# Optimization experiments

Hardware: AMD Instinct MI355X
Metric: run time of the kernel (lower is better)

## Reference

```python
import jax, jax.numpy as jnp
import numpy as np

SEQ, D, H, P, FINAL = 2048, 1024, 16, 64, 1024


def setup_inputs() -> dict:
    key = jax.random.key(0)
    k_x, k_q, k_k, k_v, k_w = jax.random.split(key, 5)
    return {
        "x": jax.random.normal(k_x, (SEQ, D), dtype=jnp.float32),
        "Qw": jax.random.uniform(k_q, (H, D, P), dtype=jnp.float32),
        "Kw": jax.random.uniform(k_k, (H, D, P), dtype=jnp.float32),
        "Vw": jax.random.uniform(k_v, (H, D, P), dtype=jnp.float32),
        "W_fin": jax.random.normal(k_w, (H * P, FINAL), dtype=jnp.float32) * (1.0 / np.sqrt(H * P)),
        "b_fin": jnp.zeros((FINAL,), dtype=jnp.float32),
    }


def reference(x, Qw, Kw, Vw, W_fin, b_fin):
    # x: [S, D]; Qw/Kw/Vw: [H, D, P]
    Q = jnp.einsum("sd,hdp->hsp", x, Qw)  # [H, S, P]
    K = jnp.einsum("sd,hdp->hsp", x, Kw)
    V = jnp.einsum("sd,hdp->hsp", x, Vw)
    p_dim = K.shape[-1]
    # sigmoid attention: no row-wise normalization, scale by P (not sqrt(P))
    score = jax.nn.sigmoid(jnp.einsum("hsp,htp->hst", Q, K) / p_dim)  # [H, S, S]
    attn = jnp.einsum("hst,htp->hsp", score, V)  # [H, S, P]
    # faithful raw reshape (torch .reshape(seq, -1) on contiguous [H, S, P])
    concat = attn.reshape(x.shape[0], -1)  # [S, H*P]
    return concat @ W_fin + b_fin  # [S, FINAL]
```

## Files before the change

### kernel.cpp

```cpp
#include <hip/hip_runtime.h>
#include <hip/hip_bf16.h>

#define SEQL 2048
#define DMODEL 1024
#define NH 16
#define HEADP 64
#define FINALD 1024

using bf16x8 = __attribute__((ext_vector_type(8))) short;
using f32x4  = __attribute__((ext_vector_type(4))) float;
using s16x4  = __attribute__((ext_vector_type(4))) short;

#define WAITV(N) asm volatile("s_waitcnt vmcnt(" #N ")" ::: "memory")

__device__ __forceinline__ f32x4 mfma16(bf16x8 a, bf16x8 b, f32x4 c) {
  return __builtin_amdgcn_mfma_f32_16x16x32_bf16(a, b, c, 0, 0, 0);
}

__device__ __forceinline__ unsigned short f2bf(float f) {
  return __builtin_bit_cast(unsigned short, __float2bfloat16(f));
}

__device__ __forceinline__ void gload16(const void* g, void* l) {
  __builtin_amdgcn_global_load_lds(
      (const __attribute__((address_space(1))) void*)g,
      (__attribute__((address_space(3))) void*)l, 16, 0, 0);
}

__global__ __launch_bounds__(256) void k_prep(
    const float* __restrict__ Qw, const float* __restrict__ Kw,
    const float* __restrict__ Vw, const float* __restrict__ Wf,
    const float* __restrict__ x,
    unsigned short* __restrict__ Wt, unsigned short* __restrict__ WfT,
    unsigned short* __restrict__ xb) {
  __shared__ float tile[64][65];
  int z = blockIdx.z;
  int t = threadIdx.x;
  if (z == 4) {
    long i0 = ((long)blockIdx.y * 16 + blockIdx.x) * 2048 + t;
#pragma unroll
    for (int k = 0; k < 8; ++k) {
      long i = i0 + k * 256;
      float4 v = reinterpret_cast<const float4*>(x)[i];
      ushort4 o;
      o.x = f2bf(v.x); o.y = f2bf(v.y); o.z = f2bf(v.z); o.w = f2bf(v.w);
      reinterpret_cast<ushort4*>(xb)[i] = o;
    }
    return;
  }
  const float* src; unsigned short* dst;
  int C, tr = blockIdx.x * 64, tc;
  if (z < 3) {
    const float* s3 = (z == 0) ? Qw : (z == 1) ? Kw : Vw;
    src = s3 + (long)blockIdx.y * 65536;
    dst = Wt + (long)z * 1048576 + (long)blockIdx.y * 65536;
    C = 64; tc = 0;
  } else {
    src = Wf; dst = WfT; C = 1024; tc = blockIdx.y * 64;
  }
  const int R = 1024;
  int r0 = t >> 4, c4 = (t & 15) * 4;
#pragma unroll
  for (int i = 0; i < 4; ++i) {
    int r = i * 16 + r0;
    float4 v = *reinterpret_cast<const float4*>(src + (long)(tr + r) * C + tc + c4);
    tile[r][c4 + 0] = v.x; tile[r][c4 + 1] = v.y;
    tile[r][c4 + 2] = v.z; tile[r][c4 + 3] = v.w;
  }
  __syncthreads();
  int r4 = (t & 15) * 4, cc0 = t >> 4;
#pragma unroll
  for (int i = 0; i < 4; ++i) {
    int c = i * 16 + cc0;
    ushort4 o;
    o.x = f2bf(tile[r4 + 0][c]); o.y = f2bf(tile[r4 + 1][c]);
    o.z = f2bf(tile[r4 + 2][c]); o.w = f2bf(tile[r4 + 3][c]);
    *reinterpret_cast<ushort4*>(dst + (long)(tc + c) * R + tr + r4) = o;
  }
}

template <int EPI>
__global__ __launch_bounds__(256) void k_gemm(
    const unsigned short* __restrict__ A,
    const unsigned short* __restrict__ Bt,
    int K,
    unsigned short* __restrict__ Qb,
    unsigned short* __restrict__ Kb,
    unsigned short* __restrict__ Vtb,
    const float* __restrict__ bias,
    float* __restrict__ outf) {
  __shared__ char lds[49152];
  int flat = blockIdx.y * 16 + blockIdx.x;
  int cpx = (gridDim.x * gridDim.y) >> 3;
  flat = (flat & 7) * cpx + (flat >> 3);
  int m0 = (flat & 15) << 7, n0 = (flat >> 4) * 64;
  int t = threadIdx.x;
  int l = t & 63, w = t >> 6;
  int r = l & 15, g = l >> 4;
  int wr = w >> 1, wc = w & 1;

  const unsigned short* Arow = A + (long)m0 * K;
  const unsigned short* Brow = Bt + (long)n0 * K;
  int rr = l >> 2;
  int c8s = (((l & 3) ^ ((l >> 3) & 3)) * 8);

  auto stage = [&](int buf, int k0) {
    char* base = lds + buf * 24576;
#pragma unroll
    for (int kk = 0; kk < 2; ++kk) {
      char* dA = base + kk * 8192 + w * 2048;
      char* dB = base + 16384 + kk * 4096 + w * 1024;
      int kc = k0 + kk * 32 + c8s;
      gload16(Arow + (long)(w * 32 + rr) * K + kc, dA);
      gload16(Arow + (long)(w * 32 + 16 + rr) * K + kc, dA + 1024);
      gload16(Brow + (long)(w * 16 + rr) * K + kc, dB);
    }
  };

  int xk = (r >> 1) & 3;
  f32x4 acc[4][2] = {};
  int cur = 0, NK = K / 64;
  stage(0, 0);
  for (int kt = 0; kt < NK; ++kt) {
    __builtin_amdgcn_s_barrier();
    if (kt + 1 < NK) {
      stage(cur ^ 1, (kt + 1) * 64);
      WAITV(6);
    } else {
      WAITV(0);
    }
    __builtin_amdgcn_s_barrier();
    __builtin_amdgcn_sched_barrier(0);
    const char* base = lds + cur * 24576;
#pragma unroll
    for (int kk = 0; kk < 2; ++kk) {
      const char* As = base + kk * 8192;
      const char* Bs = base + 16384 + kk * 4096;
      bf16x8 af[4], bb[2];
#pragma unroll
      for (int i = 0; i < 4; ++i)
        af[i] = *reinterpret_cast<const bf16x8*>(As + (wr * 64 + i * 16 + r) * 64 + ((g ^ xk) * 16));
#pragma unroll
      for (int i = 0; i < 2; ++i)
        bb[i] = *reinterpret_cast<const bf16x8*>(Bs + (wc * 32 + i * 16 + r) * 64 + ((g ^ xk) * 16));
#pragma unroll
      for (int mi = 0; mi < 4; ++mi)
#pragma unroll
        for (int ni = 0; ni < 2; ++ni)
          acc[mi][ni] = mfma16(af[mi], bb[ni], acc[mi][ni]);
    }
    cur ^= 1;
  }

  if constexpr (EPI == 0) {
    int which = n0 >> 10;
    int hb = (n0 & 1023) >> 6;
    if (which < 2) {
      unsigned short* dst = (which == 0 ? Qb : Kb) + (long)hb * SEQL * HEADP;
#pragma unroll
      for (int mi = 0; mi < 4; ++mi) {
        int s0 = m0 + wr * 64 + mi * 16 + g * 4;
#pragma unroll
        for (int ni = 0; ni < 2; ++ni) {
          int p = wc * 32 + ni * 16 + r;
#pragma unroll
          for (int v = 0; v < 4; ++v)
            dst[(long)(s0 + v) * HEADP + p] = f2bf(acc[mi][ni][v]);
        }
      }
    } else {
      unsigned short* dst = Vtb + (long)hb * HEADP * SEQL;
#pragma unroll
      for (int mi = 0; mi < 4; ++mi) {
        int s0 = m0 + wr * 64 + mi * 16 + g * 4;
#pragma unroll
        for (int ni = 0; ni < 2; ++ni) {
          int p = wc * 32 + ni * 16 + r;
          ushort4 pk;
          pk.x = f2bf(acc[mi][ni][0]); pk.y = f2bf(acc[mi][ni][1]);
          pk.z = f2bf(acc[mi][ni][2]); pk.w = f2bf(acc[mi][ni][3]);
          *reinterpret_cast<ushort4*>(dst + (long)p * SEQL + s0) = pk;
        }
      }
    }
  } else {
#pragma unroll
    for (int ni = 0; ni < 2; ++ni) {
      int c = n0 + wc * 32 + ni * 16 + r;
      float bv = bias[c];
#pragma unroll
      for (int mi = 0; mi < 4; ++mi) {
        int s0 = m0 + wr * 64 + mi * 16 + g * 4;
#pragma unroll
        for (int v = 0; v < 4; ++v)
          outf[(long)(s0 + v) * FINALD + c] = acc[mi][ni][v] + bv;
      }
    }
  }
}

__global__ __launch_bounds__(256) void k_attn(
    const unsigned short* __restrict__ Qb,
    const unsigned short* __restrict__ Kb,
    const unsigned short* __restrict__ Vtb,
    unsigned short* __restrict__ Ab) {
  __shared__ char lds[40960];
  int b = blockIdx.x;
  int xcd = b & 7, j = b >> 3;
  int h = (xcd << 1) | (j & 1);
  int sblk = j >> 1;
  int lane = threadIdx.x & 63, wave = threadIdx.x >> 6;
  int r = lane & 15, g = lane >> 4;
  int q0 = sblk * 64 + wave * 16;
  const unsigned short* Qh = Qb + ((long)h * SEQL + q0) * HEADP;
  const unsigned short* Kh = Kb + (long)h * SEQL * HEADP;
  const unsigned short* Vh = Vtb + (long)h * HEADP * SEQL;

  bf16x8 qf0 = *reinterpret_cast<const bf16x8*>(Qh + (long)r * HEADP + g * 8);
  bf16x8 qf1 = *reinterpret_cast<const bf16x8*>(Qh + (long)r * HEADP + 32 + g * 8);

  f32x4 z4 = {0.f, 0.f, 0.f, 0.f};
  f32x4 oacc[4] = {z4, z4, z4, z4};
  char* slab = lds + 32768 + wave * 2048;
  int swz = (r & 7) << 4;
  const float CLN = -0.02254211001389005f;

  int sub = lane >> 3, chunk = lane & 7;
  auto stage = [&](int buf, int t0) {
    char* kb = lds + buf * 16384 + wave * 2048;
    char* vb = kb + 8192;
#pragma unroll
    for (int jj = 0; jj < 2; ++jj) {
      int row = wave * 16 + jj * 8 + sub;
      int sw = (chunk ^ (row & 7)) * 8;
      gload16(Kh + (long)(t0 + row) * HEADP + sw, kb + jj * 1024);
      gload16(Vh + (long)row * SEQL + t0 + sw, vb + jj * 1024);
    }
  };

  int cur = 0;
  stage(0, 0);
  for (int t0 = 0; t0 < SEQL; t0 += 64) {
    __builtin_amdgcn_s_barrier();
    if (t0 + 64 < SEQL) {
      stage(cur ^ 1, t0 + 64);
      WAITV(4);
    } else {
      WAITV(0);
    }
    __builtin_amdgcn_s_barrier();
    __builtin_amdgcn_sched_barrier(0);

    const char* kb = lds + cur * 16384;
    const char* vb = kb + 8192;
    f32x4 s[4] = {z4, z4, z4, z4};
    __builtin_amdgcn_s_setprio(1);
#pragma unroll
    for (int tb = 0; tb < 4; ++tb) {
      const char* krow = kb + (tb * 16 + r) * 128;
      bf16x8 k0 = *reinterpret_cast<const bf16x8*>(krow + ((g ^ (r & 7)) * 16));
      bf16x8 k1 = *reinterpret_cast<const bf16x8*>(krow + (((4 + g) ^ (r & 7)) * 16));
      s[tb] = mfma16(k0, qf0, s[tb]);
      s[tb] = mfma16(k1, qf1, s[tb]);
    }
    __builtin_amdgcn_s_setprio(0);
#pragma unroll
    for (int tb = 0; tb < 4; ++tb) {
      s16x4 pk;
#pragma unroll
      for (int v = 0; v < 4; ++v) {
        float e = __builtin_amdgcn_exp2f(s[tb][v] * CLN);
        pk[v] = (short)f2bf(__builtin_amdgcn_rcpf(1.0f + e));
      }
      *reinterpret_cast<s16x4*>(slab + r * 128 + ((tb * 32 + g * 8) ^ swz)) = pk;
    }
    bf16x8 pa0 = *reinterpret_cast<const bf16x8*>(slab + r * 128 + ((g * 16) ^ swz));
    bf16x8 pa1 = *reinterpret_cast<const bf16x8*>(slab + r * 128 + ((64 + g * 16) ^ swz));
    __builtin_amdgcn_s_setprio(1);
#pragma unroll
    for (int nb = 0; nb < 4; ++nb) {
      const char* vrow = vb + (nb * 16 + r) * 128;
      bf16x8 v0 = *reinterpret_cast<const bf16x8*>(vrow + ((g ^ (r & 7)) * 16));
      bf16x8 v1 = *reinterpret_cast<const bf16x8*>(vrow + (((4 + g) ^ (r & 7)) * 16));
      oacc[nb] = mfma16(pa0, v0, oacc[nb]);
      oacc[nb] = mfma16(pa1, v1, oacc[nb]);
    }
    __builtin_amdgcn_s_setprio(0);
    cur ^= 1;
  }
  unsigned short* Oh = Ab + ((long)h * SEQL + q0) * HEADP;
#pragma unroll
  for (int nb = 0; nb < 4; ++nb)
#pragma unroll
    for (int v = 0; v < 4; ++v)
      Oh[(g * 4 + v) * HEADP + nb * 16 + r] = f2bf(oacc[nb][v]);
}

extern "C" void kernel_launch(void* const* d_in, const int* in_sizes, int n_in,
                              void* d_out, int out_size, void* d_ws, size_t ws_size,
                              hipStream_t stream) {
  const float* x  = (const float*)d_in[0];
  const float* Qw = (const float*)d_in[1];
  const float* Kw = (const float*)d_in[2];
  const float* Vw = (const float*)d_in[3];
  const float* Wf = (const float*)d_in[4];
  const float* bf = (const float*)d_in[5];
  float* out = (float*)d_out;

  unsigned short* ws  = (unsigned short*)d_ws;
  unsigned short* xb  = ws;
  unsigned short* Wt  = ws + 2097152;
  unsigned short* WfT = ws + 5242880;
  unsigned short* Qb  = ws + 6291456;
  unsigned short* Kb  = ws + 8388608;
  unsigned short* Vtb = ws + 10485760;
  unsigned short* Ab  = ws + 12582912;

  k_prep<<<dim3(16, 16, 5), 256, 0, stream>>>(Qw, Kw, Vw, Wf, x, Wt, WfT, xb);
  k_gemm<0><<<dim3(16, 48), 256, 0, stream>>>(xb, Wt, DMODEL, Qb, Kb, Vtb, nullptr, nullptr);
  k_attn<<<512, 256, 0, stream>>>(Qb, Kb, Vtb, Ab);
  k_gemm<1><<<dim3(16, 16), 256, 0, stream>>>(Ab, WfT, DMODEL, nullptr, nullptr, nullptr, bf, out);
}
```

Baseline: 77.72 us.

## Switch attention to 32x32x16 MFMA with register-only P via permlane32 swap

The attention kernel now uses 32x32x16 bf16 MFMAs, with waves split into two query groups and two key-parity halves. The sigmoid probabilities are packed with v_cvt_pk_bf16_f32 and redistributed across lanes with v_permlane32_swap, so the LDS round-trip slab for P is removed. The V tile layout and swizzle are changed to match the new operand layout. The two key halves are reduced through LDS at the end, which adds an epilogue sync and a reduction in exchange for fewer LDS ops and larger MFMA tiles.

```diff
diff --git a/kernel.cpp b/kernel.cpp
--- a/kernel.cpp
+++ b/kernel.cpp
@@ -9,7 +9,8 @@
 
 using bf16x8 = __attribute__((ext_vector_type(8))) short;
 using f32x4  = __attribute__((ext_vector_type(4))) float;
-using s16x4  = __attribute__((ext_vector_type(4))) short;
+using f32x16 = __attribute__((ext_vector_type(16))) float;
+using u32x4  = __attribute__((ext_vector_type(4))) unsigned;
 
 #define WAITV(N) asm volatile("s_waitcnt vmcnt(" #N ")" ::: "memory")
 
@@ -204,37 +205,44 @@
     const unsigned short* __restrict__ Kb,
     const unsigned short* __restrict__ Vtb,
     unsigned short* __restrict__ Ab) {
-  __shared__ char lds[40960];
+  __shared__ char lds[32768];
   int b = blockIdx.x;
   int xcd = b & 7, j = b >> 3;
   int h = (xcd << 1) | (j & 1);
   int sblk = j >> 1;
-  int lane = threadIdx.x & 63, wave = threadIdx.x >> 6;
-  int r = lane & 15, g = lane >> 4;
-  int q0 = sblk * 64 + wave * 16;
-  const unsigned short* Qh = Qb + ((long)h * SEQL + q0) * HEADP;
+  int q0b = sblk * 64;
+  int tid = threadIdx.x;
+  int lane = tid & 63, w = tid >> 6;
+  int lo5 = lane & 31, hi = lane >> 5;
+  int qg = w & 1, tpar = w >> 1;
   const unsigned short* Kh = Kb + (long)h * SEQL * HEADP;
   const unsigned short* Vh = Vtb + (long)h * HEADP * SEQL;
-
-  bf16x8 qf0 = *reinterpret_cast<const bf16x8*>(Qh + (long)r * HEADP + g * 8);
-  bf16x8 qf1 = *reinterpret_cast<const bf16x8*>(Qh + (long)r * HEADP + 32 + g * 8);
-
-  f32x4 z4 = {0.f, 0.f, 0.f, 0.f};
-  f32x4 oacc[4] = {z4, z4, z4, z4};
-  char* slab = lds + 32768 + wave * 2048;
-  int swz = (r & 7) << 4;
+  const unsigned short* Qrow = Qb + ((long)h * SEQL + q0b + qg * 32 + lo5) * HEADP;
+
+  bf16x8 qf[4];
+#pragma unroll
+  for (int ks = 0; ks < 4; ++ks)
+    qf[ks] = *reinterpret_cast<const bf16x8*>(Qrow + ks * 16 + hi * 8);
+
+  f32x16 zz = {};
+  f32x16 oacc[2] = {zz, zz};
   const float CLN = -0.02254211001389005f;
 
-  int sub = lane >> 3, chunk = lane & 7;
   auto stage = [&](int buf, int t0) {
-    char* kb = lds + buf * 16384 + wave * 2048;
-    char* vb = kb + 8192;
+    char* kb = lds + buf * 16384 + w * 2048;
 #pragma unroll
     for (int jj = 0; jj < 2; ++jj) {
-      int row = wave * 16 + jj * 8 + sub;
-      int sw = (chunk ^ (row & 7)) * 8;
-      gload16(Kh + (long)(t0 + row) * HEADP + sw, kb + jj * 1024);
-      gload16(Vh + (long)row * SEQL + t0 + sw, vb + jj * 1024);
+      int row = w * 16 + jj * 8 + (lane >> 3);
+      int c = (lane & 7) ^ (row & 7);
+      gload16(Kh + (long)(t0 + row) * HEADP + c * 8, kb + jj * 1024);
+    }
+    char* vb = lds + buf * 16384 + 8192 + w * 2048;
+#pragma unroll
+    for (int jj = 0; jj < 2; ++jj) {
+      int vr = w * 32 + jj * 16 + (lane >> 2);
+      int p = vr & 63, tp = vr >> 6;
+      int c = (lane & 3) ^ ((p >> 1) & 3);
+      gload16(Vh + (long)p * SEQL + t0 + tp * 32 + c * 8, vb + jj * 1024);
     }
   };
 
@@ -253,47 +261,79 @@
 
     const char* kb = lds + cur * 16384;
     const char* vb = kb + 8192;
-    f32x4 s[4] = {z4, z4, z4, z4};
+    int krow = tpar * 32 + lo5;
+
+    f32x16 s = zz;
     __builtin_amdgcn_s_setprio(1);
 #pragma unroll
-    for (int tb = 0; tb < 4; ++tb) {
-      const char* krow = kb + (tb * 16 + r) * 128;
-      bf16x8 k0 = *reinterpret_cast<const bf16x8*>(krow + ((g ^ (r & 7)) * 16));
-      bf16x8 k1 = *reinterpret_cast<const bf16x8*>(krow + (((4 + g) ^ (r & 7)) * 16));
-      s[tb] = mfma16(k0, qf0, s[tb]);
-      s[tb] = mfma16(k1, qf1, s[tb]);
+    for (int ks = 0; ks < 4; ++ks) {
+      int c = ks * 2 + hi;
+      bf16x8 kf = *reinterpret_cast<const bf16x8*>(
+          kb + krow * 128 + ((c ^ (krow & 7)) * 16));
+      s = __builtin_amdgcn_mfma_f32_32x32x16_bf16(kf, qf[ks], s, 0, 0, 0);
     }
     __builtin_amdgcn_s_setprio(0);
-#pragma unroll
-    for (int tb = 0; tb < 4; ++tb) {
-      s16x4 pk;
-#pragma unroll
-      for (int v = 0; v < 4; ++v) {
-        float e = __builtin_amdgcn_exp2f(s[tb][v] * CLN);
-        pk[v] = (short)f2bf(__builtin_amdgcn_rcpf(1.0f + e));
+
+    float p[16];
+#pragma unroll
+    for (int r = 0; r < 16; ++r) {
+      float e = __builtin_amdgcn_exp2f(s[r] * CLN);
+      p[r] = __builtin_amdgcn_rcpf(1.0f + e);
+    }
+    unsigned d[8];
+#pragma unroll
+    for (int gq = 0; gq < 2; ++gq) {
+      unsigned x1, x2, y1, y2;
+      asm("v_cvt_pk_bf16_f32 %0, %1, %2" : "=v"(x1) : "v"(p[gq*8+0]), "v"(p[gq*8+1]));
+      asm("v_cvt_pk_bf16_f32 %0, %1, %2" : "=v"(x2) : "v"(p[gq*8+2]), "v"(p[gq*8+3]));
+      asm("v_cvt_pk_bf16_f32 %0, %1, %2" : "=v"(y1) : "v"(p[gq*8+4]), "v"(p[gq*8+5]));
+      asm("v_cvt_pk_bf16_f32 %0, %1, %2" : "=v"(y2) : "v"(p[gq*8+6]), "v"(p[gq*8+7]));
+      asm volatile("v_permlane32_swap_b32 %0, %1" : "+v"(x1), "+v"(y1));
+      asm volatile("v_permlane32_swap_b32 %0, %1" : "+v"(x2), "+v"(y2));
+      d[gq*4+0] = x1; d[gq*4+1] = x2; d[gq*4+2] = y1; d[gq*4+3] = y2;
+    }
+
+    __builtin_amdgcn_s_setprio(1);
+#pragma unroll
+    for (int ts = 0; ts < 2; ++ts) {
+      u32x4 pu = {d[ts*4+0], d[ts*4+1], d[ts*4+2], d[ts*4+3]};
+      bf16x8 pa = __builtin_bit_cast(bf16x8, pu);
+#pragma unroll
+      for (int nb = 0; nb < 2; ++nb) {
+        int prow = nb * 32 + lo5;
+        int c = ts * 2 + hi;
+        bf16x8 vf = *reinterpret_cast<const bf16x8*>(
+            vb + tpar * 4096 + prow * 64 + ((c ^ ((prow >> 1) & 3)) * 16));
+        oacc[nb] = __builtin_amdgcn_mfma_f32_32x32x16_bf16(pa, vf, oacc[nb], 0, 0, 0);
       }
-      *reinterpret_cast<s16x4*>(slab + r * 128 + ((tb * 32 + g * 8) ^ swz)) = pk;
-    }
-    bf16x8 pa0 = *reinterpret_cast<const bf16x8*>(slab + r * 128 + ((g * 16) ^ swz));
-    bf16x8 pa1 = *reinterpret_cast<const bf16x8*>(slab + r * 128 + ((64 + g * 16) ^ swz));
-    __builtin_amdgcn_s_setprio(1);
-#pragma unroll
-    for (int nb = 0; nb < 4; ++nb) {
-      const char* vrow = vb + (nb * 16 + r) * 128;
-      bf16x8 v0 = *reinterpret_cast<const bf16x8*>(vrow + ((g ^ (r & 7)) * 16));
-      bf16x8 v1 = *reinterpret_cast<const bf16x8*>(vrow + (((4 + g) ^ (r & 7)) * 16));
-      oacc[nb] = mfma16(pa0, v0, oacc[nb]);
-      oacc[nb] = mfma16(pa1, v1, oacc[nb]);
     }
     __builtin_amdgcn_s_setprio(0);
     cur ^= 1;
   }
-  unsigned short* Oh = Ab + ((long)h * SEQL + q0) * HEADP;
-#pragma unroll
-  for (int nb = 0; nb < 4; ++nb)
-#pragma unroll
-    for (int v = 0; v < 4; ++v)
-      Oh[(g * 4 + v) * HEADP + nb * 16 + r] = f2bf(oacc[nb][v]);
+
+  __syncthreads();
+  float* pr = (float*)(lds + tpar * 16384);
+#pragma unroll
+  for (int nb = 0; nb < 2; ++nb)
+#pragma unroll
+    for (int r = 0; r < 16; ++r) {
+      int q = qg * 32 + (r & 3) + 8 * (r >> 2) + 4 * hi;
+      pr[q * 64 + nb * 32 + lo5] = oacc[nb][r];
+    }
+  __syncthreads();
+  int q = tid >> 2, pc = (tid & 3) * 16;
+  const float* p0 = (const float*)(lds);
+  const float* p1 = (const float*)(lds + 16384);
+  unsigned short* Oh = Ab + ((long)h * SEQL + q0b + q) * HEADP + pc;
+#pragma unroll
+  for (int k = 0; k < 4; ++k) {
+    float4 a = *reinterpret_cast<const float4*>(p0 + q * 64 + pc + k * 4);
+    float4 c = *reinterpret_cast<const float4*>(p1 + q * 64 + pc + k * 4);
+    ushort4 o;
+    o.x = f2bf(a.x + c.x); o.y = f2bf(a.y + c.y);
+    o.z = f2bf(a.z + c.z); o.w = f2bf(a.w + c.w);
+    *reinterpret_cast<ushort4*>(Oh + k * 4) = o;
+  }
 }
 
 extern "C" void kernel_launch(void* const* d_in, const int* in_sizes, int n_in,
```

New measurement: 76.82 us. About the same (-1.2%).
